# Kernel tuning notes

Measured on AMD Instinct MI355X. Metric: run time of the kernel, lower is better.

## Reference

```python
import jax, jax.numpy as jnp
import numpy as np

B, N, C = 4, 1024, 1024
H = 16
D = C // H
FF = 4 * C
EPS = 1e-5


def setup_inputs() -> dict:
    key = jax.random.key(0)
    ks = jax.random.split(key, 16)
    s = 0.02
    return {
        "x": jax.random.normal(ks[0], (B, N, C), jnp.float32),
        "c": jax.random.normal(ks[1], (B, C), jnp.float32),
        "node_mask": jax.random.randint(ks[2], (B, N), 0, 2) > 0,
        "qkv_w": jax.random.normal(ks[3], (C, 3 * C), jnp.float32) * s,
        "proj_w": jax.random.normal(ks[4], (C, C), jnp.float32) * s,
        "proj_b": jnp.zeros((C,), jnp.float32),
        "fc1_w": jax.random.normal(ks[5], (C, FF), jnp.float32) * s,
        "fc1_b": jnp.zeros((FF,), jnp.float32),
        "fc2_w": jax.random.normal(ks[6], (FF, C), jnp.float32) * s,
        "fc2_b": jnp.zeros((C,), jnp.float32),
        "ada1_w": jax.random.normal(ks[7], (C, C), jnp.float32) * s,
        "ada1_b": jnp.zeros((C,), jnp.float32),
        "ada2_w": jax.random.normal(ks[8], (C, 6 * C), jnp.float32) * s,
        "ada2_b": jnp.zeros((6 * C,), jnp.float32),
    }


def _layernorm(x):
    # LayerNorm without affine params (elementwise_affine=False), eps=1e-5
    mu = jnp.mean(x, axis=-1, keepdims=True)
    var = jnp.mean(jnp.square(x - mu), axis=-1, keepdims=True)
    return (x - mu) * jax.lax.rsqrt(var + EPS)


def _modulate(x, shift, scale):
    return x * (1.0 + scale[:, None, :]) + shift[:, None, :]


def _attention(x, node_mask, qkv_w, proj_w, proj_b):
    b, n, c = x.shape
    qkv = (x @ qkv_w).reshape(b, n, 3, H, D)
    q, k, v = jnp.moveaxis(qkv, 2, 0)          # each [b, n, H, D]
    q = q.transpose(0, 2, 1, 3)                # [b, H, n, D]
    k = k.transpose(0, 2, 1, 3)
    v = v.transpose(0, 2, 1, 3)
    scale = D ** -0.5
    scores = jnp.einsum("bhnd,bhmd->bhnm", q, k) * scale
    mask = node_mask[:, None, None, :]          # key mask [b,1,1,n]
    scores = jnp.where(mask, scores, -jnp.inf)
    attn = jax.nn.softmax(scores, axis=-1)
    out = jnp.einsum("bhnm,bhmd->bhnd", attn, v)
    out = out.transpose(0, 2, 1, 3).reshape(b, n, c)
    return out @ proj_w + proj_b


def _mlp(x, fc1_w, fc1_b, fc2_w, fc2_b):
    h = jax.nn.gelu(x @ fc1_w + fc1_b, approximate=False)
    return h @ fc2_w + fc2_b


def reference(x, c, node_mask, qkv_w, proj_w, proj_b, fc1_w, fc1_b,
              fc2_w, fc2_b, ada1_w, ada1_b, ada2_w, ada2_b):
    # adaLN: Linear -> SiLU -> Linear -> 6 chunks along feature dim
    ada = jax.nn.silu(c @ ada1_w + ada1_b) @ ada2_w + ada2_b
    (shift_msa, scale_msa, gate_msa,
     shift_mlp, scale_mlp, gate_mlp) = jnp.split(ada, 6, axis=1)

    attn_out = _attention(x, node_mask, qkv_w, proj_w, proj_b)
    x = x + gate_msa[:, None, :] * _modulate(_layernorm(attn_out), shift_msa, scale_msa)

    mlp_out = _mlp(x, fc1_w, fc1_b, fc2_w, fc2_b)
    x = x + gate_mlp[:, None, :] * _modulate(_layernorm(mlp_out), shift_mlp, scale_mlp)
    return x
```

## Files before the change

kernel.cpp:

```cpp
#include <hip/hip_runtime.h>

typedef unsigned short u16;
typedef __attribute__((ext_vector_type(8))) short short8;
typedef __attribute__((ext_vector_type(8))) unsigned short u16x8;
typedef __attribute__((ext_vector_type(4))) unsigned short u16x4;
typedef __attribute__((ext_vector_type(4))) float f32x4;

#define DEVINL __device__ __forceinline__
#define SGB0 __builtin_amdgcn_sched_barrier(0)

DEVINL u16 f2b(float f) {
    union { float f; unsigned u; } a; a.f = f;
    unsigned r = a.u + 0x7FFFu + ((a.u >> 16) & 1u);
    return (u16)(r >> 16);
}
DEVINL float b2f(u16 h) {
    union { unsigned u; float f; } a; a.u = ((unsigned)h) << 16;
    return a.f;
}

DEVINL void gload16(const void* g, void* l) {
    __builtin_amdgcn_global_load_lds(
        (const __attribute__((address_space(1))) void*)g,
        (__attribute__((address_space(3))) void*)l, 16, 0, 0);
}

__global__ void detect_mask(const unsigned char* __restrict__ m, int nbytes, int* __restrict__ flag) {
    __shared__ int any;
    if (threadIdx.x == 0) any = 0;
    __syncthreads();
    int loc = 0;
    for (int i = threadIdx.x; i < nbytes; i += 256)
        if ((i & 3) && m[i]) loc = 1;
    if (loc) atomicOr(&any, 1);
    __syncthreads();
    if (threadIdx.x == 0) *flag = any;
}

__global__ __launch_bounds__(256) void f32_to_bf16(const float* __restrict__ in, u16* __restrict__ out, int n4) {
    int i = blockIdx.x * 256 + threadIdx.x;
    if (i >= n4) return;
    float4 v = ((const float4*)in)[i];
    u16x4 o = { f2b(v.x), f2b(v.y), f2b(v.z), f2b(v.w) };
    *(u16x4*)(out + (size_t)i * 4) = o;
}

__global__ __launch_bounds__(256) void transpose_bf16(const float* __restrict__ W, u16* __restrict__ WT, int K, int N) {
    __shared__ float tile[32][33];
    int tx = threadIdx.x, ty = threadIdx.y;
    int n0 = blockIdx.x * 32, k0 = blockIdx.y * 32;
#pragma unroll
    for (int i = 0; i < 4; i++)
        tile[ty + i * 8][tx] = W[(size_t)(k0 + ty + i * 8) * N + n0 + tx];
    __syncthreads();
#pragma unroll
    for (int i = 0; i < 4; i++)
        WT[(size_t)(n0 + ty + i * 8) * K + k0 + tx] = f2b(tile[tx][ty + i * 8]);
}

__global__ __launch_bounds__(256) void transpose_v(const u16* __restrict__ qkv, u16* __restrict__ vtg) {
    __shared__ u16 tile[64][72];
    const int bh = blockIdx.x & 63, nt = blockIdx.x >> 6;
    const int b = bh >> 4, h = bh & 15;
    const int t = threadIdx.x;
    const int r = t >> 3, c = (t & 7) << 3;
#pragma unroll
    for (int i = 0; i < 2; i++) {
        int rr = r + i * 32;
        *(u16x8*)&tile[rr][c] =
            *(const u16x8*)&qkv[(size_t)(b * 1024 + nt * 64 + rr) * 3072 + 2048 + h * 64 + c];
    }
    __syncthreads();
#pragma unroll
    for (int i = 0; i < 2; i++) {
        int d = r + i * 32;
        u16x8 o;
#pragma unroll
        for (int e = 0; e < 8; e++) o[e] = tile[c + e][d];
        *(u16x8*)&vtg[(size_t)bh * 65536 + (size_t)d * 1024 + nt * 64 + c] = o;
    }
}

template <int KRLOG2>
__global__ __launch_bounds__(256) void gemv_partial(
    const float* __restrict__ h, const float* __restrict__ w,
    float* __restrict__ part, int N, int K) {
    constexpr int KR = 1 << KRLOG2;
    constexpr int KR4 = KR >> 2;
    __shared__ float hs[4 * KR];
    __shared__ float red[256 * 16];
    const int t = threadIdx.x, wv = t >> 6, l = t & 63;
    const int j4 = blockIdx.x * 256 + l * 4;
    const int kb = blockIdx.y << KRLOG2;
    for (int idx = t; idx < 4 * KR; idx += 256) {
        int b = idx >> KRLOG2, kk = idx & (KR - 1);
        hs[idx] = h[b * K + kb + kk];
    }
    __syncthreads();
    float acc[4][4];
#pragma unroll
    for (int b = 0; b < 4; b++)
#pragma unroll
        for (int c = 0; c < 4; c++) acc[b][c] = 0.f;
    const float* wp = w + (size_t)(kb + wv * KR4) * N + j4;
#pragma unroll
    for (int i = 0; i < KR4; i++) {
        float4 wf = *(const float4*)(wp + (size_t)i * N);
        int kk = wv * KR4 + i;
#pragma unroll
        for (int b = 0; b < 4; b++) {
            float hv = hs[(b << KRLOG2) + kk];
            acc[b][0] += hv * wf.x;
            acc[b][1] += hv * wf.y;
            acc[b][2] += hv * wf.z;
            acc[b][3] += hv * wf.w;
        }
    }
#pragma unroll
    for (int b = 0; b < 4; b++)
#pragma unroll
        for (int c = 0; c < 4; c++)
            red[t * 16 + b * 4 + c] = acc[b][c];
    __syncthreads();
    if (t < 64) {
#pragma unroll
        for (int b = 0; b < 4; b++) {
            float4 s;
            s.x = red[l * 16 + b * 4 + 0] + red[(l + 64) * 16 + b * 4 + 0] + red[(l + 128) * 16 + b * 4 + 0] + red[(l + 192) * 16 + b * 4 + 0];
            s.y = red[l * 16 + b * 4 + 1] + red[(l + 64) * 16 + b * 4 + 1] + red[(l + 128) * 16 + b * 4 + 1] + red[(l + 192) * 16 + b * 4 + 1];
            s.z = red[l * 16 + b * 4 + 2] + red[(l + 64) * 16 + b * 4 + 2] + red[(l + 128) * 16 + b * 4 + 2] + red[(l + 192) * 16 + b * 4 + 2];
            s.w = red[l * 16 + b * 4 + 3] + red[(l + 64) * 16 + b * 4 + 3] + red[(l + 128) * 16 + b * 4 + 3] + red[(l + 192) * 16 + b * 4 + 3];
            *(float4*)&part[(size_t)(blockIdx.y * 4 + b) * N + j4] = s;
        }
    }
}

template <int SILU>
__global__ __launch_bounds__(256) void gemv_reduce(
    const float* __restrict__ part, const float* __restrict__ bias,
    float* __restrict__ out, int N, int NK) {
    int gid = blockIdx.x * 256 + threadIdx.x;
    int b = gid / N, j = gid - b * N;
    float s = bias[j];
    for (int i = 0; i < NK; i++) s += part[(size_t)(i * 4 + b) * N + j];
    if (SILU) s = s / (1.f + __expf(-s));
    out[gid] = s;
}

template <int EPI>
__global__ __launch_bounds__(512) void gemm256(
    const u16* __restrict__ A, const u16* __restrict__ B, const float* __restrict__ bias,
    u16* __restrict__ Cb, u16* __restrict__ Cb2, int M, int N, int lda, int Ksub) {
    __shared__ u16 As[2][256 * 64];
    __shared__ u16 Bs[2][256 * 64];
    const int t = threadIdx.x;
    const int w = t >> 6, l = t & 63;
    const int l15 = l & 15, lg = l >> 4;
    const int nTN = N >> 8;
    const int ntiles = (M >> 8) * nTN;
    const int sk = blockIdx.x / ntiles;
    int tb = blockIdx.x - sk * ntiles;
    tb = (tb & 7) * (ntiles >> 3) + (tb >> 3);
    const int tm = tb / nTN, tn = tb - tm * nTN;
    const int row0 = tm << 8, col0 = tn << 8;
    const int wr = (w >> 2) << 7, wc = (w & 3) << 6;
    const int k_begin = sk * Ksub;

    const int rA = t >> 3;
    const int cswz = ((t & 7) ^ (rA & 7)) << 3;
    const u16* gA = A + (size_t)(row0 + rA) * lda + cswz + k_begin;
    const u16* gB = B + (size_t)(col0 + rA) * lda + cswz + k_begin;
    const int rsw = l15 & 7;

    f32x4 acc[8][4];
#pragma unroll
    for (int i = 0; i < 8; i++)
#pragma unroll
        for (int j = 0; j < 4; j++) acc[i][j] = (f32x4){0.f, 0.f, 0.f, 0.f};

    const int nkt = Ksub >> 6;

    auto SA = [&](int kt, int j) {
        gload16(gA + (size_t)j * 64 * lda + (kt << 6), As[kt & 1] + j * 4096 + w * 512);
    };
    auto SB = [&](int kt, int j) {
        gload16(gB + (size_t)j * 64 * lda + (kt << 6), Bs[kt & 1] + j * 4096 + w * 512);
    };

    SA(0, 0); SA(0, 2); SB(0, 0); SB(0, 1); SB(0, 2); SB(0, 3); SA(0, 1); SA(0, 3);
    SA(1, 0); SA(1, 2); SB(1, 0); SB(1, 1); SB(1, 2); SB(1, 3); SA(1, 1); SA(1, 3);

    for (int kt = 0; kt < nkt; ++kt) {
        const int cur = kt & 1;
        const bool last = (kt == nkt - 1);
        const bool stg = (kt + 2 < nkt);

        if (last) asm volatile("s_waitcnt vmcnt(2)" ::: "memory");
        else      asm volatile("s_waitcnt vmcnt(10)" ::: "memory");
        SGB0;
        __builtin_amdgcn_s_barrier();
        SGB0;
        short8 a0[2][4], b0[2][2];
#pragma unroll
        for (int ks = 0; ks < 2; ks++) {
            const int chunk = (((ks << 2) + lg) ^ rsw) << 3;
#pragma unroll
            for (int mi = 0; mi < 4; mi++)
                a0[ks][mi] = *(const short8*)&As[cur][((wr + mi * 16 + l15) << 6) + chunk];
#pragma unroll
            for (int ni = 0; ni < 2; ni++)
                b0[ks][ni] = *(const short8*)&Bs[cur][((wc + ni * 16 + l15) << 6) + chunk];
        }
        asm volatile("s_waitcnt lgkmcnt(0)" ::: "memory");
        SGB0;
        __builtin_amdgcn_s_setprio(1);
#pragma unroll
        for (int ks = 0; ks < 2; ks++)
#pragma unroll
            for (int mi = 0; mi < 4; mi++)
#pragma unroll
                for (int ni = 0; ni < 2; ni++)
                    acc[mi][ni] = __builtin_amdgcn_mfma_f32_16x16x32_bf16(a0[ks][mi], b0[ks][ni], acc[mi][ni], 0, 0, 0);
        __builtin_amdgcn_s_setprio(0);

        SGB0;
        __builtin_amdgcn_s_barrier();
        SGB0;
        short8 b1[2][2];
#pragma unroll
        for (int ks = 0; ks < 2; ks++) {
            const int chunk = (((ks << 2) + lg) ^ rsw) << 3;
#pragma unroll
            for (int ni = 0; ni < 2; ni++)
                b1[ks][ni] = *(const short8*)&Bs[cur][((wc + (ni + 2) * 16 + l15) << 6) + chunk];
        }
        if (stg) { SA(kt + 2, 0); SA(kt + 2, 2); }
        asm volatile("s_waitcnt lgkmcnt(0)" ::: "memory");
        SGB0;
        __builtin_amdgcn_s_setprio(1);
#pragma unroll
        for (int ks = 0; ks < 2; ks++)
#pragma unroll
            for (int mi = 0; mi < 4; mi++)
#pragma unroll
                for (int ni = 0; ni < 2; ni++)
                    acc[mi][ni + 2] = __builtin_amdgcn_mfma_f32_16x16x32_bf16(a0[ks][mi], b1[ks][ni], acc[mi][ni + 2], 0, 0, 0);
        __builtin_amdgcn_s_setprio(0);

        if (last)     asm volatile("s_waitcnt vmcnt(0)" ::: "memory");
        else if (stg) asm volatile("s_waitcnt vmcnt(10)" ::: "memory");
        else          asm volatile("s_waitcnt vmcnt(8)" ::: "memory");
        SGB0;
        __builtin_amdgcn_s_barrier();
        SGB0;
        short8 a1[2][4];
#pragma unroll
        for (int ks = 0; ks < 2; ks++) {
            const int chunk = (((ks << 2) + lg) ^ rsw) << 3;
#pragma unroll
            for (int mi = 0; mi < 4; mi++)
                a1[ks][mi] = *(const short8*)&As[cur][((wr + (mi + 4) * 16 + l15) << 6) + chunk];
        }
        if (stg) { SB(kt + 2, 0); SB(kt + 2, 1); SB(kt + 2, 2); SB(kt + 2, 3); }
        asm volatile("s_waitcnt lgkmcnt(0)" ::: "memory");
        SGB0;
        __builtin_amdgcn_s_setprio(1);
#pragma unroll
        for (int ks = 0; ks < 2; ks++)
#pragma unroll
            for (int mi = 0; mi < 4; mi++)
#pragma unroll
                for (int ni = 0; ni < 2; ni++)
                    acc[mi + 4][ni] = __builtin_amdgcn_mfma_f32_16x16x32_bf16(a1[ks][mi], b0[ks][ni], acc[mi + 4][ni], 0, 0, 0);
        __builtin_amdgcn_s_setprio(0);

        SGB0;
        __builtin_amdgcn_s_barrier();
        SGB0;
        if (stg) { SA(kt + 2, 1); SA(kt + 2, 3); }
        __builtin_amdgcn_s_setprio(1);
#pragma unroll
        for (int ks = 0; ks < 2; ks++)
#pragma unroll
            for (int mi = 0; mi < 4; mi++)
#pragma unroll
                for (int ni = 0; ni < 2; ni++)
                    acc[mi + 4][ni + 2] = __builtin_amdgcn_mfma_f32_16x16x32_bf16(a1[ks][mi], b1[ks][ni], acc[mi + 4][ni + 2], 0, 0, 0);
        __builtin_amdgcn_s_setprio(0);
    }

    const size_t MNsz = (size_t)M * N;
    u16* dst = (sk < 2) ? Cb + (size_t)sk * MNsz : Cb2 + (size_t)(sk - 2) * MNsz;
#pragma unroll
    for (int mi = 0; mi < 8; mi++) {
#pragma unroll
        for (int ni = 0; ni < 4; ni++) {
#pragma unroll
            for (int j = 0; j < 4; j++) {
                int r = row0 + wr + mi * 16 + (lg << 2) + j;
                int c = col0 + wc + ni * 16 + l15;
                float v = acc[mi][ni][j];
                if (EPI == 0) {
                    dst[(size_t)r * N + c] = f2b(v);
                } else {
                    float vv = v + bias[c];
                    float g = 0.5f * vv * (1.f + erff(vv * 0.70710678118f));
                    dst[(size_t)r * N + c] = f2b(g);
                }
            }
        }
    }
}

__global__ __launch_bounds__(256) void attn_kernel(
    const u16* __restrict__ qkv, const u16* __restrict__ vtg,
    const unsigned char* __restrict__ maskb,
    const int* __restrict__ flagp, u16* __restrict__ out) {
    __shared__ u16 Qs[64 * 64];
    __shared__ u16 Ks[64 * 64];
    __shared__ u16 Vt[64 * 64];
    __shared__ u16 Ps[64 * 64];
    __shared__ float maskf[64];
    __shared__ float alpha_lds[64];
    __shared__ float lst_lds[64];

    int bi = (int)blockIdx.x;
    bi = (bi & 7) * 128 + (bi >> 3);
    const int qt = bi & 15, h = (bi >> 4) & 15, b = bi >> 8;
    const int t = threadIdx.x, w = t >> 6, l = t & 63;
    const int l15 = l & 15, lg = l >> 4;
    const int rsw = l15 & 7;
    const int flag = *flagp;
    const int q0 = qt << 6;
    const int bh = b * 16 + h;

    const int sr = t >> 3, sc = t & 7;
#pragma unroll
    for (int i = 0; i < 2; i++) {
        int r = sr + i * 32;
        u16x8 v = *(const u16x8*)&qkv[(size_t)(b * 1024 + q0 + r) * 3072 + h * 64 + sc * 8];
        u16x8 o;
#pragma unroll
        for (int e = 0; e < 8; e++) o[e] = f2b(b2f(v[e]) * 0.125f);
        *(u16x8*)&Qs[r * 64 + ((sc ^ (r & 7)) << 3)] = o;
    }

    f32x4 O[4];
#pragma unroll
    for (int nd = 0; nd < 4; nd++) O[nd] = (f32x4){0.f, 0.f, 0.f, 0.f};
    float mst = -1e30f, lst = 0.f;

    u16x8 kreg[2], vreg[2];
    float mnext;
    {
#pragma unroll
        for (int i = 0; i < 2; i++) {
            kreg[i] = *(const u16x8*)&qkv[(size_t)(b * 1024 + sr + i * 32) * 3072 + h * 64 + 1024 + sc * 8];
            vreg[i] = *(const u16x8*)&vtg[(size_t)bh * 65536 + (size_t)(sr + i * 32) * 1024 + sc * 8];
        }
        int gi = b * 1024 + (t & 63);
        bool ms = flag ? (maskb[gi] != 0) : (((const int*)maskb)[gi] != 0);
        mnext = ms ? 1.f : 0.f;
    }

    for (int kt = 0; kt < 16; kt++) {
        __syncthreads();
#pragma unroll
        for (int i = 0; i < 2; i++) {
            int r = sr + i * 32;
            *(u16x8*)&Ks[r * 64 + ((sc ^ (r & 7)) << 3)] = kreg[i];
            *(u16x8*)&Vt[r * 64 + ((sc ^ (r & 7)) << 3)] = vreg[i];
        }
        if (t < 64) maskf[t] = mnext;
        __syncthreads();
        if (kt < 15) {
            const int kn = (kt + 1) << 6;
#pragma unroll
            for (int i = 0; i < 2; i++) {
                kreg[i] = *(const u16x8*)&qkv[(size_t)(b * 1024 + kn + sr + i * 32) * 3072 + h * 64 + 1024 + sc * 8];
                vreg[i] = *(const u16x8*)&vtg[(size_t)bh * 65536 + (size_t)(sr + i * 32) * 1024 + kn + sc * 8];
            }
            int gi = b * 1024 + kn + (t & 63);
            bool ms = flag ? (maskb[gi] != 0) : (((const int*)maskb)[gi] != 0);
            mnext = ms ? 1.f : 0.f;
        }

        f32x4 S[4];
#pragma unroll
        for (int mi = 0; mi < 4; mi++) S[mi] = (f32x4){0.f, 0.f, 0.f, 0.f};
        __builtin_amdgcn_s_setprio(1);
#pragma unroll
        for (int ks = 0; ks < 2; ks++) {
            const int chunk = (((ks << 2) + lg) ^ rsw) << 3;
            short8 bq = *(const short8*)&Qs[(w * 16 + l15) * 64 + chunk];
#pragma unroll
            for (int mi = 0; mi < 4; mi++) {
                short8 ak = *(const short8*)&Ks[(mi * 16 + l15) * 64 + chunk];
                S[mi] = __builtin_amdgcn_mfma_f32_16x16x32_bf16(ak, bq, S[mi], 0, 0, 0);
            }
        }
        __builtin_amdgcn_s_setprio(0);

        float pm = -1e30f;
#pragma unroll
        for (int mi = 0; mi < 4; mi++) {
            f32x4 mk = *(const f32x4*)&maskf[mi * 16 + (lg << 2)];
#pragma unroll
            for (int j = 0; j < 4; j++) {
                float xv = (mk[j] > 0.f) ? S[mi][j] : -1e30f;
                S[mi][j] = xv;
                pm = fmaxf(pm, xv);
            }
        }
        pm = fmaxf(pm, __shfl_xor(pm, 16));
        pm = fmaxf(pm, __shfl_xor(pm, 32));

        bool skip = __all(pm <= mst + 8.f);
        float alpha = 1.f;
        if (!skip) {
            float mn = fmaxf(mst, pm);
            alpha = __expf(mst - mn);
            mst = mn;
        }

        float psum = 0.f;
        const int prow = w * 16 + l15;
#pragma unroll
        for (int mi = 0; mi < 4; mi++) {
            f32x4 mk = *(const f32x4*)&maskf[mi * 16 + (lg << 2)];
            u16x4 v4;
#pragma unroll
            for (int j = 0; j < 4; j++) {
                float p = __expf(S[mi][j] - mst) * mk[j];
                psum += p;
                v4[j] = f2b(p);
            }
            int ch = ((mi * 2 + (lg >> 1)) ^ rsw);
            *(u16x4*)&Ps[prow * 64 + (ch << 3) + ((lg & 1) << 2)] = v4;
        }
        psum += __shfl_xor(psum, 16);
        psum += __shfl_xor(psum, 32);
        lst = lst * alpha + psum;

        if (!skip) {
            if (lg == 0) alpha_lds[w * 16 + l15] = alpha;
            f32x4 af = *(const f32x4*)&alpha_lds[w * 16 + (lg << 2)];
#pragma unroll
            for (int nd = 0; nd < 4; nd++)
#pragma unroll
                for (int j = 0; j < 4; j++) O[nd][j] *= af[j];
        }

        __builtin_amdgcn_s_setprio(1);
#pragma unroll
        for (int ks = 0; ks < 2; ks++) {
            const int chunk = (((ks << 2) + lg) ^ rsw) << 3;
            short8 pa = *(const short8*)&Ps[(w * 16 + l15) * 64 + chunk];
#pragma unroll
            for (int nd = 0; nd < 4; nd++) {
                short8 bv = *(const short8*)&Vt[(nd * 16 + l15) * 64 + chunk];
                O[nd] = __builtin_amdgcn_mfma_f32_16x16x32_bf16(pa, bv, O[nd], 0, 0, 0);
            }
        }
        __builtin_amdgcn_s_setprio(0);
    }

    if (lg == 0) lst_lds[w * 16 + l15] = lst;
    f32x4 lf = *(const f32x4*)&lst_lds[w * 16 + (lg << 2)];
#pragma unroll
    for (int nd = 0; nd < 4; nd++)
#pragma unroll
        for (int j = 0; j < 4; j++) {
            int r = b * 1024 + q0 + w * 16 + (lg << 2) + j;
            int c = h * 64 + nd * 16 + l15;
            out[(size_t)r * 1024 + c] = f2b(O[nd][j] / lf[j]);
        }
}

__global__ __launch_bounds__(256) void ln_mod_res4(
    const u16* __restrict__ s0, const u16* __restrict__ s1, const float* __restrict__ bias,
    const float* __restrict__ resid, const float* __restrict__ ada, int oS, int oC, int oG,
    float* __restrict__ outf, u16* __restrict__ outb) {
    __shared__ float red[8];
    const int row = blockIdx.x, t = threadIdx.x, b = row >> 10;
    const float4 bv = ((const float4*)bias)[t];
    const size_t MN = 1ull << 22;
    const u16* p0 = s0 + (size_t)row * 1024 + t * 4;
    const u16* p1 = s1 + (size_t)row * 1024 + t * 4;
    u16x4 a0 = *(const u16x4*)p0;
    u16x4 a1 = *(const u16x4*)(p0 + MN);
    u16x4 a2 = *(const u16x4*)p1;
    u16x4 a3 = *(const u16x4*)(p1 + MN);
    float4 v;
    v.x = (b2f(a0[0]) + b2f(a1[0])) + (b2f(a2[0]) + b2f(a3[0])) + bv.x;
    v.y = (b2f(a0[1]) + b2f(a1[1])) + (b2f(a2[1]) + b2f(a3[1])) + bv.y;
    v.z = (b2f(a0[2]) + b2f(a1[2])) + (b2f(a2[2]) + b2f(a3[2])) + bv.z;
    v.w = (b2f(a0[3]) + b2f(a1[3])) + (b2f(a2[3]) + b2f(a3[3])) + bv.w;
    float s = v.x + v.y + v.z + v.w;
    float q = v.x * v.x + v.y * v.y + v.z * v.z + v.w * v.w;
#pragma unroll
    for (int off = 32; off >= 1; off >>= 1) {
        s += __shfl_down(s, off);
        q += __shfl_down(q, off);
    }
    if ((t & 63) == 0) { red[(t >> 6) * 2] = s; red[(t >> 6) * 2 + 1] = q; }
    __syncthreads();
    float sum = red[0] + red[2] + red[4] + red[6];
    float sq = red[1] + red[3] + red[5] + red[7];
    float mu = sum * (1.f / 1024.f);
    float var = sq * (1.f / 1024.f) - mu * mu;
    float rinv = rsqrtf(var + 1e-5f);
    const float* ad = ada + b * 6144;
    const float4 rv = ((const float4*)(resid + (size_t)row * 1024))[t];
    const float4 sc = ((const float4*)(ad + oC))[t];
    const float4 sh = ((const float4*)(ad + oS))[t];
    const float4 gt = ((const float4*)(ad + oG))[t];
    float4 o;
    o.x = rv.x + gt.x * ((v.x - mu) * rinv * (1.f + sc.x) + sh.x);
    o.y = rv.y + gt.y * ((v.y - mu) * rinv * (1.f + sc.y) + sh.y);
    o.z = rv.z + gt.z * ((v.z - mu) * rinv * (1.f + sc.z) + sh.z);
    o.w = rv.w + gt.w * ((v.w - mu) * rinv * (1.f + sc.w) + sh.w);
    ((float4*)(outf + (size_t)row * 1024))[t] = o;
    if (outb) {
        u16x4 ob = { f2b(o.x), f2b(o.y), f2b(o.z), f2b(o.w) };
        *(u16x4*)(outb + (size_t)row * 1024 + t * 4) = ob;
    }
}

extern "C" void kernel_launch(void* const* d_in, const int* in_sizes, int n_in,
                              void* d_out, int out_size, void* d_ws, size_t ws_size,
                              hipStream_t stream) {
    (void)in_sizes; (void)n_in; (void)out_size; (void)ws_size;
    const float* x = (const float*)d_in[0];
    const float* cvec = (const float*)d_in[1];
    const unsigned char* maskb = (const unsigned char*)d_in[2];
    const float* qkv_w = (const float*)d_in[3];
    const float* proj_w = (const float*)d_in[4];
    const float* proj_b = (const float*)d_in[5];
    const float* fc1_w = (const float*)d_in[6];
    const float* fc1_b = (const float*)d_in[7];
    const float* fc2_w = (const float*)d_in[8];
    const float* fc2_b = (const float*)d_in[9];
    const float* ada1_w = (const float*)d_in[10];
    const float* ada1_b = (const float*)d_in[11];
    const float* ada2_w = (const float*)d_in[12];
    const float* ada2_b = (const float*)d_in[13];
    float* outp = (float*)d_out;

    char* ws = (char*)d_ws;
    size_t off = 0;
    auto nxt = [&](size_t bytes) { size_t r = off; off += (bytes + 255) & ~(size_t)255; return r; };
    u16* qkvwT  = (u16*)(ws + nxt(3072ull * 1024 * 2));
    u16* projwT = (u16*)(ws + nxt(1024ull * 1024 * 2));
    u16* fc1wT  = (u16*)(ws + nxt(4096ull * 1024 * 2));
    u16* fc2wT  = (u16*)(ws + nxt(1024ull * 4096 * 2));
    float* adah = (float*)(ws + nxt(4ull * 1024 * 4));
    float* ada  = (float*)(ws + nxt(4ull * 6144 * 4));
    float* part1 = (float*)(ws + nxt(32ull * 4 * 1024 * 4));
    float* part2 = (float*)(ws + nxt(8ull * 4 * 6144 * 4));
    int* flag   = (int*)(ws + nxt(256));
    u16* xbf = (u16*)(ws + nxt(4096ull * 1024 * 2));
    u16* attn_buf = xbf;
    char* regC = ws + nxt(2ull * 4096 * 1024 * 4);
    u16* qkvbf = (u16*)regC;
    u16* projpart = (u16*)regC;
    u16* hbuf = (u16*)regC;
    float* y1 = (float*)(ws + nxt(4096ull * 1024 * 4));
    u16* y1b = (u16*)(ws + nxt(4096ull * 1024 * 2));
    u16* fc2part = (u16*)(ws + nxt(2ull * 4096 * 1024 * 2));
    u16* vtg = fc2part;
    u16* fc2partB = (u16*)ws;
    const size_t MN = 4096ull * 1024;

    detect_mask<<<1, 256, 0, stream>>>(maskb, 4096, flag);
    f32_to_bf16<<<4096, 256, 0, stream>>>(x, xbf, 1048576);
    transpose_bf16<<<dim3(96, 32), dim3(32, 8), 0, stream>>>(qkv_w, qkvwT, 1024, 3072);
    transpose_bf16<<<dim3(32, 32), dim3(32, 8), 0, stream>>>(proj_w, projwT, 1024, 1024);
    transpose_bf16<<<dim3(128, 32), dim3(32, 8), 0, stream>>>(fc1_w, fc1wT, 1024, 4096);
    transpose_bf16<<<dim3(32, 128), dim3(32, 8), 0, stream>>>(fc2_w, fc2wT, 4096, 1024);

    gemv_partial<5><<<dim3(4, 32), 256, 0, stream>>>(cvec, ada1_w, part1, 1024, 1024);
    gemv_reduce<1><<<16, 256, 0, stream>>>(part1, ada1_b, adah, 1024, 32);
    gemv_partial<7><<<dim3(24, 8), 256, 0, stream>>>(adah, ada2_w, part2, 6144, 1024);
    gemv_reduce<0><<<96, 256, 0, stream>>>(part2, ada2_b, ada, 6144, 8);

    gemm256<0><<<192, 512, 0, stream>>>(xbf, qkvwT, nullptr, qkvbf, nullptr, 4096, 3072, 1024, 1024);
    transpose_v<<<1024, 256, 0, stream>>>(qkvbf, vtg);
    attn_kernel<<<1024, 256, 0, stream>>>(qkvbf, vtg, maskb, flag, attn_buf);
    gemm256<0><<<256, 512, 0, stream>>>(attn_buf, projwT, nullptr, projpart, projpart + 2 * MN,
                                        4096, 1024, 1024, 256);
    ln_mod_res4<<<4096, 256, 0, stream>>>(projpart, projpart + 2 * MN, proj_b,
                                          x, ada, 0, 1024, 2048, y1, y1b);
    gemm256<2><<<256, 512, 0, stream>>>(y1b, fc1wT, fc1_b, hbuf, nullptr, 4096, 4096, 1024, 1024);
    gemm256<0><<<256, 512, 0, stream>>>(hbuf, fc2wT, nullptr, fc2part, fc2partB, 4096, 1024, 4096, 1024);
    ln_mod_res4<<<4096, 256, 0, stream>>>(fc2part, fc2partB, fc2_b,
                                          y1, ada, 3072, 4096, 5120, outp, nullptr);
}
```

Before: 267.9 us.

## Merge prep kernels and restructure GEMM barriers to overlap LDS reads with sync

Folds the mask-detection kernel into the fp32-to-bf16 conversion launch and merges the four weight transposes into a single launch, cutting kernel launch count. In the GEMM main loop, the vmcnt wait and barrier move from the top of each iteration to its end, and barriers are placed after LDS reads are issued but before waiting on them. The aim is to overlap LDS read latency with barrier sync and reduce launch overhead. The barrier and vmcnt counts must still guard the double-buffered LDS correctly.

```diff
diff --git a/kernel.cpp b/kernel.cpp
--- a/kernel.cpp
+++ b/kernel.cpp
@@ -25,30 +25,42 @@
         (__attribute__((address_space(3))) void*)l, 16, 0, 0);
 }
 
-__global__ void detect_mask(const unsigned char* __restrict__ m, int nbytes, int* __restrict__ flag) {
-    __shared__ int any;
-    if (threadIdx.x == 0) any = 0;
-    __syncthreads();
-    int loc = 0;
-    for (int i = threadIdx.x; i < nbytes; i += 256)
-        if ((i & 3) && m[i]) loc = 1;
-    if (loc) atomicOr(&any, 1);
-    __syncthreads();
-    if (threadIdx.x == 0) *flag = any;
-}
-
-__global__ __launch_bounds__(256) void f32_to_bf16(const float* __restrict__ in, u16* __restrict__ out, int n4) {
+__global__ __launch_bounds__(256) void convert_and_mask(
+    const float* __restrict__ in, u16* __restrict__ out, int n4,
+    const unsigned char* __restrict__ m, int nbytes, int* __restrict__ flag) {
     int i = blockIdx.x * 256 + threadIdx.x;
+    if (blockIdx.x == gridDim.x - 1) {
+        __shared__ int any;
+        if (threadIdx.x == 0) any = 0;
+        __syncthreads();
+        int loc = 0;
+        for (int k = threadIdx.x; k < nbytes; k += 256)
+            if ((k & 3) && m[k]) loc = 1;
+        if (loc) atomicOr(&any, 1);
+        __syncthreads();
+        if (threadIdx.x == 0) *flag = any;
+        return;
+    }
     if (i >= n4) return;
     float4 v = ((const float4*)in)[i];
     u16x4 o = { f2b(v.x), f2b(v.y), f2b(v.z), f2b(v.w) };
     *(u16x4*)(out + (size_t)i * 4) = o;
 }
 
-__global__ __launch_bounds__(256) void transpose_bf16(const float* __restrict__ W, u16* __restrict__ WT, int K, int N) {
+__global__ __launch_bounds__(256) void transpose_all(
+    const float* __restrict__ qkvw, const float* __restrict__ projw,
+    const float* __restrict__ fc1w, const float* __restrict__ fc2w,
+    u16* __restrict__ qkvT, u16* __restrict__ projT,
+    u16* __restrict__ fc1T, u16* __restrict__ fc2T) {
     __shared__ float tile[32][33];
+    int bid = blockIdx.x;
+    const float* W; u16* WT; int K, N, bx, by;
+    if (bid < 3072)      { W = qkvw;  WT = qkvT;  K = 1024; N = 3072; bx = bid % 96;  by = bid / 96; }
+    else if (bid < 4096) { int b = bid - 3072; W = projw; WT = projT; K = 1024; N = 1024; bx = b % 32;  by = b / 32; }
+    else if (bid < 8192) { int b = bid - 4096; W = fc1w;  WT = fc1T;  K = 1024; N = 4096; bx = b % 128; by = b / 128; }
+    else                 { int b = bid - 8192; W = fc2w;  WT = fc2T;  K = 4096; N = 1024; bx = b % 32;  by = b / 32; }
     int tx = threadIdx.x, ty = threadIdx.y;
-    int n0 = blockIdx.x * 32, k0 = blockIdx.y * 32;
+    int n0 = bx * 32, k0 = by * 32;
 #pragma unroll
     for (int i = 0; i < 4; i++)
         tile[ty + i * 8][tx] = W[(size_t)(k0 + ty + i * 8) * N + n0 + tx];
@@ -189,18 +201,16 @@
 
     SA(0, 0); SA(0, 2); SB(0, 0); SB(0, 1); SB(0, 2); SB(0, 3); SA(0, 1); SA(0, 3);
     SA(1, 0); SA(1, 2); SB(1, 0); SB(1, 1); SB(1, 2); SB(1, 3); SA(1, 1); SA(1, 3);
+    asm volatile("s_waitcnt vmcnt(8)" ::: "memory");
+    SGB0;
+    __builtin_amdgcn_s_barrier();
+    SGB0;
 
     for (int kt = 0; kt < nkt; ++kt) {
         const int cur = kt & 1;
-        const bool last = (kt == nkt - 1);
         const bool stg = (kt + 2 < nkt);
-
-        if (last) asm volatile("s_waitcnt vmcnt(2)" ::: "memory");
-        else      asm volatile("s_waitcnt vmcnt(10)" ::: "memory");
-        SGB0;
-        __builtin_amdgcn_s_barrier();
-        SGB0;
-        short8 a0[2][4], b0[2][2];
+        short8 a0[2][4], b0[2][2], b1[2][2], a1[2][4];
+
 #pragma unroll
         for (int ks = 0; ks < 2; ks++) {
             const int chunk = (((ks << 2) + lg) ^ rsw) << 3;
@@ -211,6 +221,8 @@
             for (int ni = 0; ni < 2; ni++)
                 b0[ks][ni] = *(const short8*)&Bs[cur][((wc + ni * 16 + l15) << 6) + chunk];
         }
+        SGB0;
+        __builtin_amdgcn_s_barrier();
         asm volatile("s_waitcnt lgkmcnt(0)" ::: "memory");
         SGB0;
         __builtin_amdgcn_s_setprio(1);
@@ -222,11 +234,10 @@
                 for (int ni = 0; ni < 2; ni++)
                     acc[mi][ni] = __builtin_amdgcn_mfma_f32_16x16x32_bf16(a0[ks][mi], b0[ks][ni], acc[mi][ni], 0, 0, 0);
         __builtin_amdgcn_s_setprio(0);
-
         SGB0;
         __builtin_amdgcn_s_barrier();
         SGB0;
-        short8 b1[2][2];
+
 #pragma unroll
         for (int ks = 0; ks < 2; ks++) {
             const int chunk = (((ks << 2) + lg) ^ rsw) << 3;
@@ -235,6 +246,8 @@
                 b1[ks][ni] = *(const short8*)&Bs[cur][((wc + (ni + 2) * 16 + l15) << 6) + chunk];
         }
         if (stg) { SA(kt + 2, 0); SA(kt + 2, 2); }
+        SGB0;
+        __builtin_amdgcn_s_barrier();
         asm volatile("s_waitcnt lgkmcnt(0)" ::: "memory");
         SGB0;
         __builtin_amdgcn_s_setprio(1);
@@ -246,14 +259,10 @@
                 for (int ni = 0; ni < 2; ni++)
                     acc[mi][ni + 2] = __builtin_amdgcn_mfma_f32_16x16x32_bf16(a0[ks][mi], b1[ks][ni], acc[mi][ni + 2], 0, 0, 0);
         __builtin_amdgcn_s_setprio(0);
-
-        if (last)     asm volatile("s_waitcnt vmcnt(0)" ::: "memory");
-        else if (stg) asm volatile("s_waitcnt vmcnt(10)" ::: "memory");
-        else          asm volatile("s_waitcnt vmcnt(8)" ::: "memory");
         SGB0;
         __builtin_amdgcn_s_barrier();
         SGB0;
-        short8 a1[2][4];
+
 #pragma unroll
         for (int ks = 0; ks < 2; ks++) {
             const int chunk = (((ks << 2) + lg) ^ rsw) << 3;
@@ -262,6 +271,8 @@
                 a1[ks][mi] = *(const short8*)&As[cur][((wr + (mi + 4) * 16 + l15) << 6) + chunk];
         }
         if (stg) { SB(kt + 2, 0); SB(kt + 2, 1); SB(kt + 2, 2); SB(kt + 2, 3); }
+        SGB0;
+        __builtin_amdgcn_s_barrier();
         asm volatile("s_waitcnt lgkmcnt(0)" ::: "memory");
         SGB0;
         __builtin_amdgcn_s_setprio(1);
@@ -273,10 +284,10 @@
                 for (int ni = 0; ni < 2; ni++)
                     acc[mi + 4][ni] = __builtin_amdgcn_mfma_f32_16x16x32_bf16(a1[ks][mi], b0[ks][ni], acc[mi + 4][ni], 0, 0, 0);
         __builtin_amdgcn_s_setprio(0);
-
         SGB0;
         __builtin_amdgcn_s_barrier();
         SGB0;
+
         if (stg) { SA(kt + 2, 1); SA(kt + 2, 3); }
         __builtin_amdgcn_s_setprio(1);
 #pragma unroll
@@ -287,6 +298,13 @@
                 for (int ni = 0; ni < 2; ni++)
                     acc[mi + 4][ni + 2] = __builtin_amdgcn_mfma_f32_16x16x32_bf16(a1[ks][mi], b1[ks][ni], acc[mi + 4][ni + 2], 0, 0, 0);
         __builtin_amdgcn_s_setprio(0);
+        if (kt + 1 < nkt) {
+            if (stg) asm volatile("s_waitcnt vmcnt(8)" ::: "memory");
+            else     asm volatile("s_waitcnt vmcnt(0)" ::: "memory");
+            SGB0;
+            __builtin_amdgcn_s_barrier();
+            SGB0;
+        }
     }
 
     const size_t MNsz = (size_t)M * N;
@@ -572,12 +590,9 @@
     u16* fc2partB = (u16*)ws;
     const size_t MN = 4096ull * 1024;
 
-    detect_mask<<<1, 256, 0, stream>>>(maskb, 4096, flag);
-    f32_to_bf16<<<4096, 256, 0, stream>>>(x, xbf, 1048576);
-    transpose_bf16<<<dim3(96, 32), dim3(32, 8), 0, stream>>>(qkv_w, qkvwT, 1024, 3072);
-    transpose_bf16<<<dim3(32, 32), dim3(32, 8), 0, stream>>>(proj_w, projwT, 1024, 1024);
-    transpose_bf16<<<dim3(128, 32), dim3(32, 8), 0, stream>>>(fc1_w, fc1wT, 1024, 4096);
-    transpose_bf16<<<dim3(32, 128), dim3(32, 8), 0, stream>>>(fc2_w, fc2wT, 4096, 1024);
+    convert_and_mask<<<4097, 256, 0, stream>>>(x, xbf, 1048576, maskb, 4096, flag);
+    transpose_all<<<12288, dim3(32, 8), 0, stream>>>(qkv_w, proj_w, fc1_w, fc2_w,
+                                                     qkvwT, projwT, fc1wT, fc2wT);
 
     gemv_partial<5><<<dim3(4, 32), 256, 0, stream>>>(cvec, ada1_w, part1, 1024, 1024);
     gemv_reduce<1><<<16, 256, 0, stream>>>(part1, ada1_b, adah, 1024, 32);
```

New measurement: 262.7 us. No clear change (-1.9%).
